# Performance work log

Hardware: AMD Instinct MI355X
Metric: run time of the kernel (lower is better)

The kernel has to match this reference:

```python
import jax, jax.numpy as jnp
import numpy as np

N_NODES = 50000   # n_nodes (adjacency is [N,N])
NNZ = 800000      # nonzeros per support (avg degree 16)
S = 3             # number of supports
D_IN = 512
D_OUT = 256


def setup_inputs() -> dict:
    key = jax.random.key(0)
    k0, k1, k2, k3, k4, k5 = jax.random.split(key, 6)
    x = jax.random.normal(k0, (N_NODES, D_IN), dtype=jnp.float32)
    # glorot-uniform per-support weights, stacked [S, D_IN, D_OUT]
    scale = float(np.sqrt(6.0 / (D_IN + D_OUT)))
    W = jax.random.uniform(k1, (S, D_IN, D_OUT), dtype=jnp.float32, minval=-scale, maxval=scale)
    rows = jax.random.randint(k2, (S, NNZ), 0, N_NODES, dtype=jnp.int32)
    cols = jax.random.randint(k3, (S, NNZ), 0, N_NODES, dtype=jnp.int32)
    vals = jax.random.uniform(k4, (S, NNZ), dtype=jnp.float32)
    # Conv1d(in=S, out=1, k=1, bias=False) == learned weighted sum over supports
    cw = jax.random.normal(k5, (S,), dtype=jnp.float32) * 0.5
    return {"x": x, "W": W, "rows": rows, "cols": cols, "vals": vals, "cw": cw}


def reference(x, W, rows, cols, vals, cw):
    # mod='output': out = relu( sum_i cw[i] * (A_i @ (x @ W_i)) )
    def spmm(r, c, v, pre):
        # A in COO: out[r] += v * pre[c]
        msgs = v[:, None] * pre[c]          # [NNZ, D_OUT] gather
        return jax.ops.segment_sum(msgs, r, num_segments=N_NODES)

    out = jnp.zeros((N_NODES, D_OUT), dtype=x.dtype)
    for i in range(S):                      # small fixed support count
        pre = x @ W[i]                      # dense GEMM [N, D_OUT]
        out = out + cw[i] * spmm(rows[i], cols[i], vals[i], pre)
    return jax.nn.relu(out)
```

## Files before the change

kernel.cpp:

```cpp
#include <hip/hip_runtime.h>
#include <stdint.h>

#define N_NODES 50000
#define N_PAD   50048
#define NNZ     800000
#define SUP     3
#define D_IN    512
#define D_OUT   256
#define TOT_E   (SUP * NNZ)
#define NBUCK   391
#define CAP     6976
#define CHUNK   3072
#define NBB     782
#define NCB     37
#define NBIN    (128 * NCB)
#define NB_WPREP 1536
#define NB_XPREP 12500
#define NB_GEMM  2346

typedef __attribute__((ext_vector_type(8))) short bf16x8;
typedef __attribute__((ext_vector_type(4))) float f32x4;
typedef __attribute__((address_space(3))) unsigned int lds_u32_t;
typedef const __attribute__((address_space(1))) unsigned int glb_u32_t;

static __device__ __forceinline__ unsigned short f2bf(float f) {
    unsigned int u = __float_as_uint(f);
    unsigned int r = (u + 0x7fffu + ((u >> 16) & 1u)) >> 16;
    return (unsigned short)r;
}
static __device__ __forceinline__ unsigned int pack_bf2(float lo, float hi) {
    unsigned int a = __float_as_uint(lo) + 0x8000u;
    unsigned int b = __float_as_uint(hi) + 0x8000u;
    return (a >> 16) | (b & 0xffff0000u);
}
static __device__ __forceinline__ float bf2f(unsigned short h) {
    return __uint_as_float(((unsigned int)h) << 16);
}
static __device__ __forceinline__ int2 ldnt_int2(const int2* p) {
    long long v = __builtin_nontemporal_load((const long long*)p);
    int2 r;
    r.x = (int)(v & 0xffffffffLL);
    r.y = (int)(v >> 32);
    return r;
}

__global__ __launch_bounds__(256) void prep_kernel(const float* __restrict__ x,
                                                   unsigned int* __restrict__ xb,
                                                   const float* __restrict__ W,
                                                   unsigned short* __restrict__ Wt) {
    const int blk = blockIdx.x;
    const int tid = threadIdx.x;
    if (blk < NB_XPREP) {
        int idx = blk * 256 + tid;
        const f32x4* src = (const f32x4*)(x) + idx * 2;
        f32x4 f0 = __builtin_nontemporal_load(src);
        f32x4 f1 = __builtin_nontemporal_load(src + 1);
        uint4 o;
        o.x = pack_bf2(f0.x, f0.y);
        o.y = pack_bf2(f0.z, f0.w);
        o.z = pack_bf2(f1.x, f1.y);
        o.w = pack_bf2(f1.z, f1.w);
        *((uint4*)xb + idx) = o;
    } else {
        int idx = (blk - NB_XPREP) * 256 + tid;
        int n = idx & (D_OUT - 1);
        int k = (idx >> 8) & (D_IN - 1);
        int s = idx >> 17;
        Wt[((size_t)s * D_OUT + n) * D_IN + k] = f2bf(W[idx]);
    }
}

__global__ __launch_bounds__(256) void bucket_kernel(const int* __restrict__ rows,
                                                     const int* __restrict__ cols,
                                                     const float* __restrict__ vals,
                                                     const float* __restrict__ cw,
                                                     int* __restrict__ bucket_cursor,
                                                     int2* __restrict__ buck) {
    __shared__ double smem8[4750];
    char* smem = (char*)smem8;
    const int blk = blockIdx.x;
    const int tid = threadIdx.x;

    int2* stage = (int2*)smem;
    unsigned short* bucket_of = (unsigned short*)(smem + 24576);
    int* hist   = (int*)(smem + 30720);
    int* sc     = hist + NBUCK;
    int* sstart = sc + 256;
    int* lcur   = sstart + NBUCK;
    int* gbase  = lcur + NBUCK;

    const int base_n = blk * CHUNK;
    const int count = min(CHUNK, TOT_E - base_n);
    float cw0 = cw[0], cw1 = cw[1], cw2 = cw[2];

    for (int i = tid; i < NBUCK; i += 256) hist[i] = 0;
    __syncthreads();
    for (int i = tid; i < count; i += 256)
        atomicAdd(&hist[rows[base_n + i] >> 7], 1);
    __syncthreads();
    int b0 = 2 * tid, b1 = b0 + 1;
    int h0 = (b0 < NBUCK) ? hist[b0] : 0;
    int h1 = (b1 < NBUCK) ? hist[b1] : 0;
    sc[tid] = h0 + h1;
    __syncthreads();
    for (int off = 1; off < 256; off <<= 1) {
        int t = (tid >= off) ? sc[tid - off] : 0;
        __syncthreads();
        sc[tid] += t;
        __syncthreads();
    }
    int excl = sc[tid] - (h0 + h1);
    if (b0 < NBUCK) { sstart[b0] = excl;      lcur[b0] = excl; }
    if (b1 < NBUCK) { sstart[b1] = excl + h0; lcur[b1] = excl + h0; }
    for (int i = tid; i < NBUCK; i += 256)
        gbase[i] = atomicAdd(&bucket_cursor[i], hist[i]);
    __syncthreads();
    for (int i = tid; i < count; i += 256) {
        int n = base_n + i;
        int r = rows[n];
        int c = __builtin_nontemporal_load(&cols[n]);
        float v = __builtin_nontemporal_load(&vals[n]);
        int s = n / NNZ;
        float w = v * (s == 0 ? cw0 : (s == 1 ? cw1 : cw2));
        int b = r >> 7;
        int p = atomicAdd(&lcur[b], 1);
        stage[p] = make_int2(((r & 127) << 18) | (s * N_NODES + c), __float_as_int(w));
        bucket_of[p] = (unsigned short)b;
    }
    __syncthreads();
    for (int i = tid; i < count; i += 256) {
        int b = bucket_of[i];
        int local_off = i - sstart[b];
        buck[(size_t)b * CAP + gbase[b] + local_off] = stage[i];
    }
}

__global__ __launch_bounds__(256) void sort_kernel(const int2* __restrict__ buck,
                                                   const int* __restrict__ bucket_cursor,
                                                   int2* __restrict__ cv,
                                                   int* __restrict__ base,
                                                   int* __restrict__ cnt) {
    __shared__ double smem8[9537];
    char* smem = (char*)smem8;
    const int tid = threadIdx.x;

    int2* stage   = (int2*)smem;
    int* hist     = (int*)(smem + 55808);
    int* sc       = hist + NBIN;
    int* rowstart = sc + 256;

    const int b = blockIdx.x;
    const int sz = bucket_cursor[b];
    const int2* src = buck + (size_t)b * CAP;

    for (int i = tid; i < NBIN; i += 256) hist[i] = 0;
    __syncthreads();
    for (int i = tid; i < sz; i += 256) {
        int key = src[i].x;
        int bin = (key >> 18) * NCB + ((key & 0x3FFFF) >> 12);
        atomicAdd(&hist[bin], 1);
    }
    __syncthreads();
    const int lo = tid * 19;
    const int hi = min(lo + 19, NBIN);
    int acc = 0;
    for (int i = lo; i < hi; ++i) acc += hist[i];
    sc[tid] = acc;
    __syncthreads();
    for (int off = 1; off < 256; off <<= 1) {
        int t = (tid >= off) ? sc[tid - off] : 0;
        __syncthreads();
        sc[tid] += t;
        __syncthreads();
    }
    int run = sc[tid] - acc;
    for (int i = lo; i < hi; ++i) {
        int h = hist[i];
        hist[i] = run;
        run += h;
    }
    __syncthreads();
    if (tid < 128) rowstart[tid] = hist[tid * NCB];
    if (tid == 0)  rowstart[128] = sz;
    __syncthreads();
    for (int i = tid; i < sz; i += 256) {
        int2 e = src[i];
        int key = e.x;
        int bin = (key >> 18) * NCB + ((key & 0x3FFFF) >> 12);
        int p = atomicAdd(&hist[bin], 1);
        stage[p] = make_int2(key & 0x3FFFF, e.y);
    }
    __syncthreads();
    size_t gb = (size_t)b * CAP;
    for (int i = tid; i < sz; i += 256) cv[gb + i] = stage[i];
    int r = b * 128 + tid;
    if (tid < 128 && r < N_NODES) {
        base[r] = (int)gb + rowstart[tid];
        cnt[r]  = rowstart[tid + 1] - rowstart[tid];
    }
}

__global__ __launch_bounds__(256) void gemm_kernel(const unsigned short* __restrict__ xb,
                                                   const unsigned short* __restrict__ Wt,
                                                   unsigned short* __restrict__ pre) {
    __shared__ unsigned short lds_a[128 * 64];
    __shared__ unsigned short lds_b[128 * 64];
    const int blk = blockIdx.x;
    const int tid = threadIdx.x;

    constexpr int SWQ = NB_GEMM / 8;
    constexpr int SWR = NB_GEMM % 8;
    const int xcd = blk & 7, pos = blk >> 3;
    const int my = (xcd < SWR ? xcd * (SWQ + 1)
                              : SWR * (SWQ + 1) + (xcd - SWR) * SWQ) + pos;
    const int mt  = my / 6;
    const int rem = my % 6;
    const int m0 = mt * 128;
    const int n0 = (rem & 1) * 128;
    const int s  = rem >> 1;
    const unsigned short* wt = Wt + (size_t)s * D_OUT * D_IN;
    const int wave = tid >> 6;
    const int lane = tid & 63;
    const int quad = lane >> 4;
    const int lo   = lane & 15;
    const int wm = (wave & 1) * 64;
    const int wn = (wave >> 1) * 64;

    f32x4 acc[4][4] = {};

    for (int kb = 0; kb < D_IN; kb += 64) {
        __syncthreads();
        #pragma unroll
        for (int c = 0; c < 4; ++c) {
            int idx = c * 256 + tid;
            int row = idx >> 3;
            int kp  = idx & 7;
            const unsigned short* ga = xb + (size_t)(m0 + row) * D_IN + kb + kp * 8;
            __builtin_amdgcn_global_load_lds((glb_u32_t*)ga,
                                             (lds_u32_t*)&lds_a[idx * 8], 16, 0, 0);
            const unsigned short* gb = wt + (size_t)(n0 + row) * D_IN + kb + kp * 8;
            __builtin_amdgcn_global_load_lds((glb_u32_t*)gb,
                                             (lds_u32_t*)&lds_b[idx * 8], 16, 0, 0);
        }
        __syncthreads();

        #pragma unroll
        for (int t = 0; t < 2; ++t) {
            bf16x8 af[4], bfr[4];
            #pragma unroll
            for (int i = 0; i < 4; ++i)
                af[i] = *(const bf16x8*)&lds_a[(wm + 16 * i + lo) * 64 + t * 32 + quad * 8];
            #pragma unroll
            for (int j = 0; j < 4; ++j)
                bfr[j] = *(const bf16x8*)&lds_b[(wn + 16 * j + lo) * 64 + t * 32 + quad * 8];
            #pragma unroll
            for (int i = 0; i < 4; ++i)
                #pragma unroll
                for (int j = 0; j < 4; ++j)
                    acc[i][j] = __builtin_amdgcn_mfma_f32_16x16x32_bf16(af[i], bfr[j], acc[i][j], 0, 0, 0);
        }
    }

    #pragma unroll
    for (int i = 0; i < 4; ++i) {
        #pragma unroll
        for (int j = 0; j < 4; ++j) {
            int gn = n0 + wn + 16 * j + lo;
            #pragma unroll
            for (int r = 0; r < 4; ++r) {
                int gm2 = m0 + wm + 16 * i + quad * 4 + r;
                if (gm2 < N_NODES)
                    pre[((size_t)s * N_NODES + gm2) * D_OUT + gn] = f2bf(acc[i][j][r]);
            }
        }
    }
}

__global__ __launch_bounds__(256) void spmm_kernel(const unsigned short* __restrict__ pre,
                                                   const int* __restrict__ base,
                                                   const int* __restrict__ cnt,
                                                   const int2* __restrict__ cv,
                                                   float* __restrict__ out) {
    int row  = blockIdx.x * 4 + (threadIdx.x >> 6);
    int lane = threadIdx.x & 63;
    int start = base[row];
    int end   = start + cnt[row];
    float a0 = 0.f, a1 = 0.f, a2 = 0.f, a3 = 0.f;
    int j = start;
    for (; j + 8 <= end; j += 8) {
        int2 e[8];
        #pragma unroll
        for (int q = 0; q < 8; ++q) e[q] = ldnt_int2(&cv[j + q]);
        ushort4 p[8];
        #pragma unroll
        for (int q = 0; q < 8; ++q)
            p[q] = *(const ushort4*)(pre + (size_t)e[q].x * D_OUT + lane * 4);
        #pragma unroll
        for (int q = 0; q < 8; ++q) {
            float w = __int_as_float(e[q].y);
            a0 += w * bf2f(p[q].x);
            a1 += w * bf2f(p[q].y);
            a2 += w * bf2f(p[q].z);
            a3 += w * bf2f(p[q].w);
        }
    }
    for (; j + 4 <= end; j += 4) {
        int2 e[4];
        #pragma unroll
        for (int q = 0; q < 4; ++q) e[q] = ldnt_int2(&cv[j + q]);
        ushort4 p[4];
        #pragma unroll
        for (int q = 0; q < 4; ++q)
            p[q] = *(const ushort4*)(pre + (size_t)e[q].x * D_OUT + lane * 4);
        #pragma unroll
        for (int q = 0; q < 4; ++q) {
            float w = __int_as_float(e[q].y);
            a0 += w * bf2f(p[q].x);
            a1 += w * bf2f(p[q].y);
            a2 += w * bf2f(p[q].z);
            a3 += w * bf2f(p[q].w);
        }
    }
    for (; j < end; ++j) {
        int2 e = ldnt_int2(&cv[j]);
        float w = __int_as_float(e.y);
        ushort4 p = *(const ushort4*)(pre + (size_t)e.x * D_OUT + lane * 4);
        a0 += w * bf2f(p.x);
        a1 += w * bf2f(p.y);
        a2 += w * bf2f(p.z);
        a3 += w * bf2f(p.w);
    }
    f32x4 o;
    o.x = fmaxf(a0, 0.f);
    o.y = fmaxf(a1, 0.f);
    o.z = fmaxf(a2, 0.f);
    o.w = fmaxf(a3, 0.f);
    __builtin_nontemporal_store(o, (f32x4*)(out + (size_t)row * D_OUT + lane * 4));
}

extern "C" void kernel_launch(void* const* d_in, const int* in_sizes, int n_in,
                              void* d_out, int out_size, void* d_ws, size_t ws_size,
                              hipStream_t stream) {
    const float* x    = (const float*)d_in[0];
    const float* W    = (const float*)d_in[1];
    const int*   rows = (const int*)d_in[2];
    const int*   cols = (const int*)d_in[3];
    const float* vals = (const float*)d_in[4];
    const float* cw   = (const float*)d_in[5];
    float* out = (float*)d_out;

    char* ws = (char*)d_ws;
    size_t off = 0;
    auto alloc = [&](size_t bytes) -> void* {
        void* p = ws + off;
        off += (bytes + 255) & ~(size_t)255;
        return p;
    };
    unsigned short* pre  = (unsigned short*)alloc((size_t)SUP * N_NODES * D_OUT * 2);
    unsigned short* xb   = (unsigned short*)alloc((size_t)N_PAD * D_IN * 2);
    unsigned short* Wt   = (unsigned short*)alloc((size_t)SUP * D_OUT * D_IN * 2);
    int* base            = (int*)alloc((size_t)N_NODES * 4);
    int* cnt             = (int*)alloc((size_t)N_NODES * 4);
    int* bucket_cursor   = (int*)alloc((size_t)NBUCK * 4);
    int2* cv             = (int2*)alloc((size_t)NBUCK * CAP * 8);
    int2* buck           = (int2*)d_out;

    hipMemsetAsync(bucket_cursor, 0, (size_t)NBUCK * 4, stream);

    bucket_kernel<<<NBB, 256, 0, stream>>>(rows, cols, vals, cw, bucket_cursor, buck);
    prep_kernel<<<NB_XPREP + NB_WPREP, 256, 0, stream>>>(x, (unsigned int*)xb, W, Wt);
    sort_kernel<<<NBUCK, 256, 0, stream>>>(buck, bucket_cursor, cv, base, cnt);
    gemm_kernel<<<NB_GEMM, 256, 0, stream>>>(xb, Wt, pre);
    spmm_kernel<<<N_NODES / 4, 256, 0, stream>>>(pre, base, cnt, cv, out);
}
```

Baseline: 481.4 us.

## Process multiple rows per wave in column-block order for gather locality

Switches the SpMM from one wave per row to a persistent grid where each wave owns about nine consecutive rows. The wave walks the 37 column blocks in order and, for each row, consumes only the edges whose column falls in the current block, so concurrent gathers from the pre matrix hit a narrower address range and reuse L2. This relies on the edges within a row already being sorted by column. The cost is serialized per-edge loads with no unrolling, less memory-level parallelism per wave, and uneven work across waves.

Result: slower. 897.5 us (+86.4%).

```diff
diff --git a/kernel.cpp b/kernel.cpp
--- a/kernel.cpp
+++ b/kernel.cpp
@@ -17,6 +17,9 @@
 #define NB_WPREP 1536
 #define NB_XPREP 12500
 #define NB_GEMM  2346
+#define SPMM_NB  1536
+#define NWAVES   (SPMM_NB * 4)
+#define ROWS_PW  9
 
 typedef __attribute__((ext_vector_type(8))) short bf16x8;
 typedef __attribute__((ext_vector_type(4))) float f32x4;
@@ -276,66 +279,62 @@
     }
 }
 
-__global__ __launch_bounds__(256) void spmm_kernel(const unsigned short* __restrict__ pre,
-                                                   const int* __restrict__ base,
-                                                   const int* __restrict__ cnt,
-                                                   const int2* __restrict__ cv,
-                                                   float* __restrict__ out) {
-    int row  = blockIdx.x * 4 + (threadIdx.x >> 6);
-    int lane = threadIdx.x & 63;
-    int start = base[row];
-    int end   = start + cnt[row];
-    float a0 = 0.f, a1 = 0.f, a2 = 0.f, a3 = 0.f;
-    int j = start;
-    for (; j + 8 <= end; j += 8) {
-        int2 e[8];
+__global__ __launch_bounds__(256, 6) void spmm_kernel(const unsigned short* __restrict__ pre,
+                                                      const int* __restrict__ base,
+                                                      const int* __restrict__ cnt,
+                                                      const int2* __restrict__ cv,
+                                                      float* __restrict__ out) {
+    const int wid  = blockIdx.x * 4 + (threadIdx.x >> 6);
+    const int lane = threadIdx.x & 63;
+    const int rs = (int)(((long)wid * N_NODES) / NWAVES);
+    const int re = (int)(((long)(wid + 1) * N_NODES) / NWAVES);
+
+    int j[ROWS_PW], je[ROWS_PW];
+    f32x4 acc[ROWS_PW];
+    #pragma unroll
+    for (int r = 0; r < ROWS_PW; ++r) {
+        int row = rs + r;
+        bool v = row < re;
+        int b = v ? base[row] : 0;
+        j[r]  = b;
+        je[r] = v ? b + cnt[row] : b;
+        acc[r].x = 0.f; acc[r].y = 0.f; acc[r].z = 0.f; acc[r].w = 0.f;
+    }
+
+    const unsigned short* prel = pre + lane * 4;
+
+    for (int cb = 0; cb < NCB; ++cb) {
         #pragma unroll
-        for (int q = 0; q < 8; ++q) e[q] = ldnt_int2(&cv[j + q]);
-        ushort4 p[8];
-        #pragma unroll
-        for (int q = 0; q < 8; ++q)
-            p[q] = *(const ushort4*)(pre + (size_t)e[q].x * D_OUT + lane * 4);
-        #pragma unroll
-        for (int q = 0; q < 8; ++q) {
-            float w = __int_as_float(e[q].y);
-            a0 += w * bf2f(p[q].x);
-            a1 += w * bf2f(p[q].y);
-            a2 += w * bf2f(p[q].z);
-            a3 += w * bf2f(p[q].w);
-        }
-    }
-    for (; j + 4 <= end; j += 4) {
-        int2 e[4];
-        #pragma unroll
-        for (int q = 0; q < 4; ++q) e[q] = ldnt_int2(&cv[j + q]);
-        ushort4 p[4];
-        #pragma unroll
-        for (int q = 0; q < 4; ++q)
-            p[q] = *(const ushort4*)(pre + (size_t)e[q].x * D_OUT + lane * 4);
-        #pragma unroll
-        for (int q = 0; q < 4; ++q) {
-            float w = __int_as_float(e[q].y);
-            a0 += w * bf2f(p[q].x);
-            a1 += w * bf2f(p[q].y);
-            a2 += w * bf2f(p[q].z);
-            a3 += w * bf2f(p[q].w);
-        }
-    }
-    for (; j < end; ++j) {
-        int2 e = ldnt_int2(&cv[j]);
-        float w = __int_as_float(e.y);
-        ushort4 p = *(const ushort4*)(pre + (size_t)e.x * D_OUT + lane * 4);
-        a0 += w * bf2f(p.x);
-        a1 += w * bf2f(p.y);
-        a2 += w * bf2f(p.z);
-        a3 += w * bf2f(p.w);
-    }
-    f32x4 o;
-    o.x = fmaxf(a0, 0.f);
-    o.y = fmaxf(a1, 0.f);
-    o.z = fmaxf(a2, 0.f);
-    o.w = fmaxf(a3, 0.f);
-    __builtin_nontemporal_store(o, (f32x4*)(out + (size_t)row * D_OUT + lane * 4));
+        for (int r = 0; r < ROWS_PW; ++r) {
+            int jj = j[r];
+            const int end = je[r];
+            while (jj < end) {
+                int2 e = ldnt_int2(&cv[jj]);
+                if ((e.x >> 12) != cb) break;
+                float w = __int_as_float(e.y);
+                ushort4 p = *(const ushort4*)(prel + (size_t)e.x * D_OUT);
+                acc[r].x += w * bf2f(p.x);
+                acc[r].y += w * bf2f(p.y);
+                acc[r].z += w * bf2f(p.z);
+                acc[r].w += w * bf2f(p.w);
+                ++jj;
+            }
+            j[r] = jj;
+        }
+    }
+
+    #pragma unroll
+    for (int r = 0; r < ROWS_PW; ++r) {
+        int row = rs + r;
+        if (row < re) {
+            f32x4 o;
+            o.x = fmaxf(acc[r].x, 0.f);
+            o.y = fmaxf(acc[r].y, 0.f);
+            o.z = fmaxf(acc[r].z, 0.f);
+            o.w = fmaxf(acc[r].w, 0.f);
+            __builtin_nontemporal_store(o, (f32x4*)(out + (size_t)row * D_OUT + lane * 4));
+        }
+    }
 }
 
 extern "C" void kernel_launch(void* const* d_in, const int* in_sizes, int n_in,
@@ -371,5 +370,5 @@
     prep_kernel<<<NB_XPREP + NB_WPREP, 256, 0, stream>>>(x, (unsigned int*)xb, W, Wt);
     sort_kernel<<<NBUCK, 256, 0, stream>>>(buck, bucket_cursor, cv, base, cnt);
     gemm_kernel<<<NB_GEMM, 256, 0, stream>>>(xb, Wt, pre);
-    spmm_kernel<<<N_NODES / 4, 256, 0, stream>>>(pre, base, cnt, cv, out);
-}
+    spmm_kernel<<<SPMM_NB, 256, 0, stream>>>(pre, base, cnt, cv, out);
+}
```

## Fuse bucket with prep and sort with GEMM, use 64-row buckets

Applied to the files above, without the earlier changes.

Merges the edge-bucketing kernel with the x/W bf16 conversion into one launch, and the per-bucket sort with the dense GEMM into another, so independent work shares a grid and fewer launches and tail gaps remain. Buckets shrink to 64 rows, so the sort only needs a 64-bin histogram by local row instead of a row×column-chunk binning, which drops the column-chunk ordering inside each row. The SpMM inner loop gains a 16-wide unrolled gather stage for more memory-level parallelism. The risks are larger shared-memory footprints lowering occupancy for the light prep blocks, a possible loss of gather locality without column ordering, and more registers in the SpMM.

Result: no change. 477.7 us (-0.8%).

```diff
diff --git a/kernel.cpp b/kernel.cpp
--- a/kernel.cpp
+++ b/kernel.cpp
@@ -8,12 +8,10 @@
 #define D_IN    512
 #define D_OUT   256
 #define TOT_E   (SUP * NNZ)
-#define NBUCK   391
-#define CAP     6976
+#define NBUCK   782
+#define CAP     3680
 #define CHUNK   3072
 #define NBB     782
-#define NCB     37
-#define NBIN    (128 * NCB)
 #define NB_WPREP 1536
 #define NB_XPREP 12500
 #define NB_GEMM  2346
@@ -44,14 +42,82 @@
     return r;
 }
 
-__global__ __launch_bounds__(256) void prep_kernel(const float* __restrict__ x,
-                                                   unsigned int* __restrict__ xb,
-                                                   const float* __restrict__ W,
-                                                   unsigned short* __restrict__ Wt) {
+__global__ __launch_bounds__(256) void prepbucket_kernel(const int* __restrict__ rows,
+                                                         const int* __restrict__ cols,
+                                                         const float* __restrict__ vals,
+                                                         const float* __restrict__ cw,
+                                                         int* __restrict__ bucket_cursor,
+                                                         int2* __restrict__ buck,
+                                                         const float* __restrict__ x,
+                                                         unsigned int* __restrict__ xb,
+                                                         const float* __restrict__ W,
+                                                         unsigned short* __restrict__ Wt) {
+    __shared__ double smem8[5536];
+    char* smem = (char*)smem8;
     const int blk = blockIdx.x;
     const int tid = threadIdx.x;
-    if (blk < NB_XPREP) {
-        int idx = blk * 256 + tid;
+
+    if (blk < NBB) {
+        int2* stage = (int2*)smem;
+        unsigned short* bucket_of = (unsigned short*)(smem + 24576);
+        int* hist   = (int*)(smem + 30720);
+        int* sc     = (int*)(smem + 33848);
+        int* sstart = (int*)(smem + 34872);
+        int* lcur   = (int*)(smem + 38000);
+        int* gbase  = (int*)(smem + 41128);
+
+        const int base_n = blk * CHUNK;
+        const int count = min(CHUNK, TOT_E - base_n);
+        float cw0 = cw[0], cw1 = cw[1], cw2 = cw[2];
+
+        for (int i = tid; i < NBUCK; i += 256) hist[i] = 0;
+        __syncthreads();
+        for (int i = tid; i < count; i += 256)
+            atomicAdd(&hist[rows[base_n + i] >> 6], 1);
+        __syncthreads();
+        const int lo = tid * 4;
+        const int hi = min(lo + 4, NBUCK);
+        int acc = 0;
+        for (int i = lo; i < hi; ++i) acc += hist[i];
+        sc[tid] = acc;
+        __syncthreads();
+        for (int off = 1; off < 256; off <<= 1) {
+            int t = (tid >= off) ? sc[tid - off] : 0;
+            __syncthreads();
+            sc[tid] += t;
+            __syncthreads();
+        }
+        int run = sc[tid] - acc;
+        for (int i = lo; i < hi; ++i) {
+            int h = hist[i];
+            sstart[i] = run;
+            lcur[i]   = run;
+            run += h;
+        }
+        __syncthreads();
+        for (int i = tid; i < NBUCK; i += 256)
+            gbase[i] = atomicAdd(&bucket_cursor[i], hist[i]);
+        __syncthreads();
+        for (int i = tid; i < count; i += 256) {
+            int n = base_n + i;
+            int r = rows[n];
+            int c = __builtin_nontemporal_load(&cols[n]);
+            float v = __builtin_nontemporal_load(&vals[n]);
+            int s = n / NNZ;
+            float w = v * (s == 0 ? cw0 : (s == 1 ? cw1 : cw2));
+            int b = r >> 6;
+            int p = atomicAdd(&lcur[b], 1);
+            stage[p] = make_int2(((r & 63) << 18) | (s * N_NODES + c), __float_as_int(w));
+            bucket_of[p] = (unsigned short)b;
+        }
+        __syncthreads();
+        for (int i = tid; i < count; i += 256) {
+            int b = bucket_of[i];
+            int local_off = i - sstart[b];
+            buck[(size_t)b * CAP + gbase[b] + local_off] = stage[i];
+        }
+    } else if (blk < NBB + NB_XPREP) {
+        int idx = (blk - NBB) * 256 + tid;
         const f32x4* src = (const f32x4*)(x) + idx * 2;
         f32x4 f0 = __builtin_nontemporal_load(src);
         f32x4 f1 = __builtin_nontemporal_load(src + 1);
@@ -62,7 +128,7 @@
         o.w = pack_bf2(f1.z, f1.w);
         *((uint4*)xb + idx) = o;
     } else {
-        int idx = (blk - NB_XPREP) * 256 + tid;
+        int idx = (blk - NBB - NB_XPREP) * 256 + tid;
         int n = idx & (D_OUT - 1);
         int k = (idx >> 8) & (D_IN - 1);
         int s = idx >> 17;
@@ -70,207 +136,131 @@
     }
 }
 
-__global__ __launch_bounds__(256) void bucket_kernel(const int* __restrict__ rows,
-                                                     const int* __restrict__ cols,
-                                                     const float* __restrict__ vals,
-                                                     const float* __restrict__ cw,
-                                                     int* __restrict__ bucket_cursor,
-                                                     int2* __restrict__ buck) {
-    __shared__ double smem8[4750];
+__global__ __launch_bounds__(256) void sortgemm_kernel(const int2* __restrict__ buck,
+                                                       const int* __restrict__ bucket_cursor,
+                                                       int2* __restrict__ cv,
+                                                       int* __restrict__ base,
+                                                       int* __restrict__ cnt,
+                                                       const unsigned short* __restrict__ xb,
+                                                       const unsigned short* __restrict__ Wt,
+                                                       unsigned short* __restrict__ pre) {
+    __shared__ double smem8[4096];
     char* smem = (char*)smem8;
     const int blk = blockIdx.x;
     const int tid = threadIdx.x;
 
-    int2* stage = (int2*)smem;
-    unsigned short* bucket_of = (unsigned short*)(smem + 24576);
-    int* hist   = (int*)(smem + 30720);
-    int* sc     = hist + NBUCK;
-    int* sstart = sc + 256;
-    int* lcur   = sstart + NBUCK;
-    int* gbase  = lcur + NBUCK;
-
-    const int base_n = blk * CHUNK;
-    const int count = min(CHUNK, TOT_E - base_n);
-    float cw0 = cw[0], cw1 = cw[1], cw2 = cw[2];
-
-    for (int i = tid; i < NBUCK; i += 256) hist[i] = 0;
-    __syncthreads();
-    for (int i = tid; i < count; i += 256)
-        atomicAdd(&hist[rows[base_n + i] >> 7], 1);
-    __syncthreads();
-    int b0 = 2 * tid, b1 = b0 + 1;
-    int h0 = (b0 < NBUCK) ? hist[b0] : 0;
-    int h1 = (b1 < NBUCK) ? hist[b1] : 0;
-    sc[tid] = h0 + h1;
-    __syncthreads();
-    for (int off = 1; off < 256; off <<= 1) {
-        int t = (tid >= off) ? sc[tid - off] : 0;
-        __syncthreads();
-        sc[tid] += t;
-        __syncthreads();
-    }
-    int excl = sc[tid] - (h0 + h1);
-    if (b0 < NBUCK) { sstart[b0] = excl;      lcur[b0] = excl; }
-    if (b1 < NBUCK) { sstart[b1] = excl + h0; lcur[b1] = excl + h0; }
-    for (int i = tid; i < NBUCK; i += 256)
-        gbase[i] = atomicAdd(&bucket_cursor[i], hist[i]);
-    __syncthreads();
-    for (int i = tid; i < count; i += 256) {
-        int n = base_n + i;
-        int r = rows[n];
-        int c = __builtin_nontemporal_load(&cols[n]);
-        float v = __builtin_nontemporal_load(&vals[n]);
-        int s = n / NNZ;
-        float w = v * (s == 0 ? cw0 : (s == 1 ? cw1 : cw2));
-        int b = r >> 7;
-        int p = atomicAdd(&lcur[b], 1);
-        stage[p] = make_int2(((r & 127) << 18) | (s * N_NODES + c), __float_as_int(w));
-        bucket_of[p] = (unsigned short)b;
-    }
-    __syncthreads();
-    for (int i = tid; i < count; i += 256) {
-        int b = bucket_of[i];
-        int local_off = i - sstart[b];
-        buck[(size_t)b * CAP + gbase[b] + local_off] = stage[i];
-    }
-}
-
-__global__ __launch_bounds__(256) void sort_kernel(const int2* __restrict__ buck,
-                                                   const int* __restrict__ bucket_cursor,
-                                                   int2* __restrict__ cv,
-                                                   int* __restrict__ base,
-                                                   int* __restrict__ cnt) {
-    __shared__ double smem8[9537];
-    char* smem = (char*)smem8;
-    const int tid = threadIdx.x;
-
-    int2* stage   = (int2*)smem;
-    int* hist     = (int*)(smem + 55808);
-    int* sc       = hist + NBIN;
-    int* rowstart = sc + 256;
-
-    const int b = blockIdx.x;
-    const int sz = bucket_cursor[b];
-    const int2* src = buck + (size_t)b * CAP;
-
-    for (int i = tid; i < NBIN; i += 256) hist[i] = 0;
-    __syncthreads();
-    for (int i = tid; i < sz; i += 256) {
-        int key = src[i].x;
-        int bin = (key >> 18) * NCB + ((key & 0x3FFFF) >> 12);
-        atomicAdd(&hist[bin], 1);
-    }
-    __syncthreads();
-    const int lo = tid * 19;
-    const int hi = min(lo + 19, NBIN);
-    int acc = 0;
-    for (int i = lo; i < hi; ++i) acc += hist[i];
-    sc[tid] = acc;
-    __syncthreads();
-    for (int off = 1; off < 256; off <<= 1) {
-        int t = (tid >= off) ? sc[tid - off] : 0;
-        __syncthreads();
-        sc[tid] += t;
-        __syncthreads();
-    }
-    int run = sc[tid] - acc;
-    for (int i = lo; i < hi; ++i) {
-        int h = hist[i];
-        hist[i] = run;
-        run += h;
-    }
-    __syncthreads();
-    if (tid < 128) rowstart[tid] = hist[tid * NCB];
-    if (tid == 0)  rowstart[128] = sz;
-    __syncthreads();
-    for (int i = tid; i < sz; i += 256) {
-        int2 e = src[i];
-        int key = e.x;
-        int bin = (key >> 18) * NCB + ((key & 0x3FFFF) >> 12);
-        int p = atomicAdd(&hist[bin], 1);
-        stage[p] = make_int2(key & 0x3FFFF, e.y);
-    }
-    __syncthreads();
-    size_t gb = (size_t)b * CAP;
-    for (int i = tid; i < sz; i += 256) cv[gb + i] = stage[i];
-    int r = b * 128 + tid;
-    if (tid < 128 && r < N_NODES) {
-        base[r] = (int)gb + rowstart[tid];
-        cnt[r]  = rowstart[tid + 1] - rowstart[tid];
-    }
-}
-
-__global__ __launch_bounds__(256) void gemm_kernel(const unsigned short* __restrict__ xb,
-                                                   const unsigned short* __restrict__ Wt,
-                                                   unsigned short* __restrict__ pre) {
-    __shared__ unsigned short lds_a[128 * 64];
-    __shared__ unsigned short lds_b[128 * 64];
-    const int blk = blockIdx.x;
-    const int tid = threadIdx.x;
-
-    constexpr int SWQ = NB_GEMM / 8;
-    constexpr int SWR = NB_GEMM % 8;
-    const int xcd = blk & 7, pos = blk >> 3;
-    const int my = (xcd < SWR ? xcd * (SWQ + 1)
-                              : SWR * (SWQ + 1) + (xcd - SWR) * SWQ) + pos;
-    const int mt  = my / 6;
-    const int rem = my % 6;
-    const int m0 = mt * 128;
-    const int n0 = (rem & 1) * 128;
-    const int s  = rem >> 1;
-    const unsigned short* wt = Wt + (size_t)s * D_OUT * D_IN;
-    const int wave = tid >> 6;
-    const int lane = tid & 63;
-    const int quad = lane >> 4;
-    const int lo   = lane & 15;
-    const int wm = (wave & 1) * 64;
-    const int wn = (wave >> 1) * 64;
-
-    f32x4 acc[4][4] = {};
-
-    for (int kb = 0; kb < D_IN; kb += 64) {
-        __syncthreads();
-        #pragma unroll
-        for (int c = 0; c < 4; ++c) {
-            int idx = c * 256 + tid;
-            int row = idx >> 3;
-            int kp  = idx & 7;
-            const unsigned short* ga = xb + (size_t)(m0 + row) * D_IN + kb + kp * 8;
-            __builtin_amdgcn_global_load_lds((glb_u32_t*)ga,
-                                             (lds_u32_t*)&lds_a[idx * 8], 16, 0, 0);
-            const unsigned short* gb = wt + (size_t)(n0 + row) * D_IN + kb + kp * 8;
-            __builtin_amdgcn_global_load_lds((glb_u32_t*)gb,
-                                             (lds_u32_t*)&lds_b[idx * 8], 16, 0, 0);
-        }
-        __syncthreads();
-
-        #pragma unroll
-        for (int t = 0; t < 2; ++t) {
-            bf16x8 af[4], bfr[4];
+    if (blk < NBUCK) {
+        int2* stage = (int2*)smem;
+        int* hist   = (int*)(smem + 29440);
+        int* sc     = (int*)(smem + 29696);
+        int* sstart = (int*)(smem + 29952);
+        int* cur    = (int*)(smem + 30208);
+
+        const int b = blk;
+        const int sz = bucket_cursor[b];
+        const int2* src = buck + (size_t)b * CAP;
+
+        if (tid < 64) hist[tid] = 0;
+        __syncthreads();
+        for (int i = tid; i < sz; i += 256)
+            atomicAdd(&hist[((unsigned)src[i].x) >> 18], 1);
+        __syncthreads();
+        if (tid < 64) sc[tid] = hist[tid];
+        __syncthreads();
+        for (int off = 1; off < 64; off <<= 1) {
+            int t = (tid >= off && tid < 64) ? sc[tid - off] : 0;
+            __syncthreads();
+            if (tid < 64) sc[tid] += t;
+            __syncthreads();
+        }
+        if (tid < 64) {
+            int st = sc[tid] - hist[tid];
+            sstart[tid] = st;
+            cur[tid] = st;
+        }
+        __syncthreads();
+        for (int i = tid; i < sz; i += 256) {
+            int2 e = src[i];
+            int rl = ((unsigned)e.x) >> 18;
+            int p = atomicAdd(&cur[rl], 1);
+            stage[p] = make_int2(e.x & 0x3FFFF, e.y);
+        }
+        __syncthreads();
+        size_t gb = (size_t)b * CAP;
+        for (int i = tid; i < sz; i += 256) cv[gb + i] = stage[i];
+        int r = b * 64 + tid;
+        if (tid < 64 && r < N_NODES) {
+            base[r] = (int)gb + sstart[tid];
+            cnt[r]  = hist[tid];
+        }
+    } else {
+        unsigned short* lds_a = (unsigned short*)smem;
+        unsigned short* lds_b = (unsigned short*)(smem + 16384);
+        const int gblk = blk - NBUCK;
+        constexpr int SWQ = NB_GEMM / 8;
+        constexpr int SWR = NB_GEMM % 8;
+        const int xcd = gblk & 7, pos = gblk >> 3;
+        const int my = (xcd < SWR ? xcd * (SWQ + 1)
+                                  : SWR * (SWQ + 1) + (xcd - SWR) * SWQ) + pos;
+        const int mt  = my / 6;
+        const int rem = my % 6;
+        const int m0 = mt * 128;
+        const int n0 = (rem & 1) * 128;
+        const int s  = rem >> 1;
+        const unsigned short* wt = Wt + (size_t)s * D_OUT * D_IN;
+        const int wave = tid >> 6;
+        const int lane = tid & 63;
+        const int quad = lane >> 4;
+        const int lo   = lane & 15;
+        const int wm = (wave & 1) * 64;
+        const int wn = (wave >> 1) * 64;
+
+        f32x4 acc[4][4] = {};
+
+        for (int kb = 0; kb < D_IN; kb += 64) {
+            __syncthreads();
             #pragma unroll
-            for (int i = 0; i < 4; ++i)
-                af[i] = *(const bf16x8*)&lds_a[(wm + 16 * i + lo) * 64 + t * 32 + quad * 8];
+            for (int c = 0; c < 4; ++c) {
+                int idx = c * 256 + tid;
+                int row = idx >> 3;
+                int kp  = idx & 7;
+                const unsigned short* ga = xb + (size_t)(m0 + row) * D_IN + kb + kp * 8;
+                __builtin_amdgcn_global_load_lds((glb_u32_t*)ga,
+                                                 (lds_u32_t*)&lds_a[idx * 8], 16, 0, 0);
+                const unsigned short* gb = wt + (size_t)(n0 + row) * D_IN + kb + kp * 8;
+                __builtin_amdgcn_global_load_lds((glb_u32_t*)gb,
+                                                 (lds_u32_t*)&lds_b[idx * 8], 16, 0, 0);
+            }
+            __syncthreads();
+
             #pragma unroll
-            for (int j = 0; j < 4; ++j)
-                bfr[j] = *(const bf16x8*)&lds_b[(wn + 16 * j + lo) * 64 + t * 32 + quad * 8];
-            #pragma unroll
-            for (int i = 0; i < 4; ++i)
+            for (int t = 0; t < 2; ++t) {
+                bf16x8 af[4], bfr[4];
+                #pragma unroll
+                for (int i = 0; i < 4; ++i)
+                    af[i] = *(const bf16x8*)&lds_a[(wm + 16 * i + lo) * 64 + t * 32 + quad * 8];
                 #pragma unroll
                 for (int j = 0; j < 4; ++j)
-                    acc[i][j] = __builtin_amdgcn_mfma_f32_16x16x32_bf16(af[i], bfr[j], acc[i][j], 0, 0, 0);
-        }
-    }
-
-    #pragma unroll
-    for (int i = 0; i < 4; ++i) {
-        #pragma unroll
-        for (int j = 0; j < 4; ++j) {
-            int gn = n0 + wn + 16 * j + lo;
+                    bfr[j] = *(const bf16x8*)&lds_b[(wn + 16 * j + lo) * 64 + t * 32 + quad * 8];
+                #pragma unroll
+                for (int i = 0; i < 4; ++i)
+                    #pragma unroll
+                    for (int j = 0; j < 4; ++j)
+                        acc[i][j] = __builtin_amdgcn_mfma_f32_16x16x32_bf16(af[i], bfr[j], acc[i][j], 0, 0, 0);
+            }
+        }
+
+        #pragma unroll
+        for (int i = 0; i < 4; ++i) {
             #pragma unroll
-            for (int r = 0; r < 4; ++r) {
-                int gm2 = m0 + wm + 16 * i + quad * 4 + r;
-                if (gm2 < N_NODES)
-                    pre[((size_t)s * N_NODES + gm2) * D_OUT + gn] = f2bf(acc[i][j][r]);
+            for (int j = 0; j < 4; ++j) {
+                int gn = n0 + wn + 16 * j + lo;
+                #pragma unroll
+                for (int r = 0; r < 4; ++r) {
+                    int gm2 = m0 + wm + 16 * i + quad * 4 + r;
+                    if (gm2 < N_NODES)
+                        pre[((size_t)s * N_NODES + gm2) * D_OUT + gn] = f2bf(acc[i][j][r]);
+                }
             }
         }
     }
@@ -287,6 +277,23 @@
     int end   = start + cnt[row];
     float a0 = 0.f, a1 = 0.f, a2 = 0.f, a3 = 0.f;
     int j = start;
+    for (; j + 16 <= end; j += 16) {
+        int2 e[16];
+        #pragma unroll
+        for (int q = 0; q < 16; ++q) e[q] = ldnt_int2(&cv[j + q]);
+        ushort4 p[16];
+        #pragma unroll
+        for (int q = 0; q < 16; ++q)
+            p[q] = *(const ushort4*)(pre + (size_t)e[q].x * D_OUT + lane * 4);
+        #pragma unroll
+        for (int q = 0; q < 16; ++q) {
+            float w = __int_as_float(e[q].y);
+            a0 += w * bf2f(p[q].x);
+            a1 += w * bf2f(p[q].y);
+            a2 += w * bf2f(p[q].z);
+            a3 += w * bf2f(p[q].w);
+        }
+    }
     for (; j + 8 <= end; j += 8) {
         int2 e[8];
         #pragma unroll
@@ -367,9 +374,9 @@
 
     hipMemsetAsync(bucket_cursor, 0, (size_t)NBUCK * 4, stream);
 
-    bucket_kernel<<<NBB, 256, 0, stream>>>(rows, cols, vals, cw, bucket_cursor, buck);
-    prep_kernel<<<NB_XPREP + NB_WPREP, 256, 0, stream>>>(x, (unsigned int*)xb, W, Wt);
-    sort_kernel<<<NBUCK, 256, 0, stream>>>(buck, bucket_cursor, cv, base, cnt);
-    gemm_kernel<<<NB_GEMM, 256, 0, stream>>>(xb, Wt, pre);
+    prepbucket_kernel<<<NBB + NB_XPREP + NB_WPREP, 256, 0, stream>>>(
+        rows, cols, vals, cw, bucket_cursor, buck, x, (unsigned int*)xb, W, Wt);
+    sortgemm_kernel<<<NBUCK + NB_GEMM, 256, 0, stream>>>(
+        buck, bucket_cursor, cv, base, cnt, xb, Wt, pre);
     spmm_kernel<<<N_NODES / 4, 256, 0, stream>>>(pre, base, cnt, cv, out);
 }
```
